# Performance work log

Hardware: AMD Instinct MI355X
Metric: run time of the kernel (lower is better)

## Reference

```python
import math
import jax, jax.numpy as jnp
import numpy as np

B, V, N, D = 256, 16, 1024, 512
CLIP = 10.0


def setup_inputs() -> dict:
    key = jax.random.key(0)
    ks = jax.random.split(key, 9)
    s = 0.02
    return {
        "g_node": jax.random.normal(ks[0], (B, D), jnp.float32),
        "Z_veh": jax.random.normal(ks[1], (B, V, D), jnp.float32),
        "g_graph": jax.random.normal(ks[2], (B, D), jnp.float32),
        "Z_node": jax.random.normal(ks[3], (B, N, D), jnp.float32),
        "mask": jax.random.randint(ks[4], (B, N), 0, 2).astype(bool),
        "W_ctx": jax.random.normal(ks[5], (D, 3 * D), jnp.float32) * s,
        "b_ctx": jnp.zeros((D,), jnp.float32),
        "Wq": jax.random.normal(ks[6], (D, D), jnp.float32) * s,
        "Wk": jax.random.normal(ks[7], (D, D), jnp.float32) * s,
    }


def reference(g_node, Z_veh, g_graph, Z_node, mask, W_ctx, b_ctx, Wq, Wk):
    scale = math.sqrt(Z_node.shape[-1])
    # concat -> Linear(3D, D) -> ReLU   (torch Linear: x @ W.T + b)
    cat = jnp.concatenate([g_node, Z_veh.mean(axis=1), g_graph], axis=-1)  # [B,3D]
    ctx = jax.nn.relu(cat @ W_ctx.T + b_ctx)  # [B,D]
    Q = ctx @ Wq.T  # [B,D]
    K = jnp.einsum("bnd,ed->bne", Z_node, Wk)  # [B,N,D]
    logits = jnp.einsum("bd,bnd->bn", Q, K) / scale  # [B,N]
    logits = CLIP * jnp.tanh(logits)
    logits = jnp.where(mask, logits, -jnp.inf)
    return logits
```

## Files before the change

### kernel.cpp

```cpp
#include <hip/hip_runtime.h>
#include <math.h>

#define Bz  256
#define Vz  16
#define Nz  1024
#define Dz  512
#define TD  1536
#define INV_SCALE 0.04419417382415922f
#define MASKED_VAL -1.0e30f

__global__ __launch_bounds__(256) void k0_zm(const float* __restrict__ Z_veh,
                                             float* __restrict__ Zm)
{
    const int idx = blockIdx.x * 256 + threadIdx.x;
    const int b   = idx >> 7;
    const int d4  = (idx & 127) * 4;
    const float* p = Z_veh + (size_t)b * Vz * Dz + d4;
    float4 s = {0.f, 0.f, 0.f, 0.f};
#pragma unroll
    for (int v = 0; v < Vz; ++v) {
        float4 t = *(const float4*)(p + (size_t)v * Dz);
        s.x += t.x; s.y += t.y; s.z += t.z; s.w += t.w;
    }
    s.x *= 0.0625f; s.y *= 0.0625f; s.z *= 0.0625f; s.w *= 0.0625f;
    *(float4*)&Zm[(size_t)b * Dz + d4] = s;
}

__global__ __launch_bounds__(256) void kA(const float* __restrict__ g_node,
                                          const float* __restrict__ Zm,
                                          const float* __restrict__ g_graph,
                                          const float* __restrict__ W_ctx,
                                          const float* __restrict__ Wq,
                                          const float* __restrict__ Wk,
                                          float* __restrict__ Cp2,
                                          float* __restrict__ GP)
{
    __shared__ float As[16][64];
    __shared__ float Bs[16][64];
    const int tid = threadIdx.x;
    const int tm = tid >> 4;
    const int tn = tid & 15;
    float acc[4][4] = {};

    if (blockIdx.x < 256) {
        const int idx = blockIdx.x;
        const int m0 = (idx >> 5) * 64;
        const int n0 = ((idx >> 3) & 3) * 64;
        const int kz = idx & 7;

        for (int kt = 0; kt < 192; kt += 16) {
            const int k0   = kz * 192 + kt;
            const int reg  = k0 >> 9;
            const int kloc = k0 & 511;
            const int ar = tid >> 2, ac = (tid & 3) * 4;
            float4 va = *(const float4*)&W_ctx[(size_t)(m0 + ar) * TD + k0 + ac];
            const int br = tid >> 2, bc = (tid & 3) * 4;
            const float* bsrc = (reg == 0) ? g_node : (reg == 2) ? g_graph : Zm;
            float4 vb = *(const float4*)&bsrc[(size_t)(n0 + br) * Dz + kloc + bc];
            __syncthreads();
            As[ac + 0][ar] = va.x; As[ac + 1][ar] = va.y;
            As[ac + 2][ar] = va.z; As[ac + 3][ar] = va.w;
            Bs[bc + 0][br] = vb.x; Bs[bc + 1][br] = vb.y;
            Bs[bc + 2][br] = vb.z; Bs[bc + 3][br] = vb.w;
            __syncthreads();
#pragma unroll
            for (int kk = 0; kk < 16; ++kk) {
                float4 a  = *(const float4*)&As[kk][tm * 4];
                float4 bb = *(const float4*)&Bs[kk][tn * 4];
                float av[4] = {a.x, a.y, a.z, a.w};
                float bv[4] = {bb.x, bb.y, bb.z, bb.w};
#pragma unroll
                for (int i = 0; i < 4; ++i)
#pragma unroll
                    for (int j = 0; j < 4; ++j)
                        acc[i][j] += av[i] * bv[j];
            }
        }
#pragma unroll
        for (int i = 0; i < 4; ++i) {
            float4 v = {acc[i][0], acc[i][1], acc[i][2], acc[i][3]};
            *(float4*)&Cp2[((size_t)kz * Dz + m0 + tm * 4 + i) * Bz + n0 + tn * 4] = v;
        }
    } else {
        const int g  = blockIdx.x - 256;
        const int m0 = (g >> 5) * 64;
        const int n0 = ((g >> 2) & 7) * 64;
        const int kz = g & 3;

        for (int kt = 0; kt < 128; kt += 16) {
            const int k0 = kz * 128 + kt;
            const int r = tid >> 4, c = (tid & 15) * 4;
            float4 va = *(const float4*)&Wq[(size_t)(k0 + r) * Dz + m0 + c];
            float4 vb = *(const float4*)&Wk[(size_t)(k0 + r) * Dz + n0 + c];
            __syncthreads();
            *(float4*)&As[r][c] = va;
            *(float4*)&Bs[r][c] = vb;
            __syncthreads();
#pragma unroll
            for (int kk = 0; kk < 16; ++kk) {
                float4 a  = *(const float4*)&As[kk][tm * 4];
                float4 bb = *(const float4*)&Bs[kk][tn * 4];
                float av[4] = {a.x, a.y, a.z, a.w};
                float bv[4] = {bb.x, bb.y, bb.z, bb.w};
#pragma unroll
                for (int i = 0; i < 4; ++i)
#pragma unroll
                    for (int j = 0; j < 4; ++j)
                        acc[i][j] += av[i] * bv[j];
            }
        }
#pragma unroll
        for (int i = 0; i < 4; ++i) {
            float4 v = {acc[i][0], acc[i][1], acc[i][2], acc[i][3]};
            *(float4*)&GP[((size_t)kz * Dz + m0 + tm * 4 + i) * Dz + n0 + tn * 4] = v;
        }
    }
}

__global__ __launch_bounds__(256) void kB(const float* __restrict__ Cp2,
                                          const float* __restrict__ bias,
                                          const float* __restrict__ GP,
                                          float* __restrict__ QkP)
{
    __shared__ float As[16][64];
    __shared__ float Bs[16][64];
    const int m0 = blockIdx.x * 64;
    const int n0 = blockIdx.y * 64;
    const int kz = blockIdx.z;
    const int tid = threadIdx.x;
    const int tm = tid >> 4, tn = tid & 15;

    float acc[4][4] = {};
    for (int kt = 0; kt < 64; kt += 16) {
        const int k0 = kz * 64 + kt;
        const int r = tid >> 4, col = (tid & 15) * 4;
        float4 s = {0.f, 0.f, 0.f, 0.f};
#pragma unroll
        for (int z = 0; z < 8; ++z) {
            float4 p = *(const float4*)&Cp2[((size_t)z * Dz + k0 + r) * Bz + m0 + col];
            s.x += p.x; s.y += p.y; s.z += p.z; s.w += p.w;
        }
        const float bv = bias[k0 + r];
        s.x = fmaxf(s.x + bv, 0.f); s.y = fmaxf(s.y + bv, 0.f);
        s.z = fmaxf(s.z + bv, 0.f); s.w = fmaxf(s.w + bv, 0.f);
        float4 t = {0.f, 0.f, 0.f, 0.f};
#pragma unroll
        for (int z = 0; z < 4; ++z) {
            float4 p = *(const float4*)&GP[((size_t)z * Dz + k0 + r) * Dz + n0 + col];
            t.x += p.x; t.y += p.y; t.z += p.z; t.w += p.w;
        }
        __syncthreads();
        *(float4*)&As[r][col] = s;
        *(float4*)&Bs[r][col] = t;
        __syncthreads();
#pragma unroll
        for (int kk = 0; kk < 16; ++kk) {
            float4 a  = *(const float4*)&As[kk][tm * 4];
            float4 bb = *(const float4*)&Bs[kk][tn * 4];
            float av[4] = {a.x, a.y, a.z, a.w};
            float bv2[4] = {bb.x, bb.y, bb.z, bb.w};
#pragma unroll
            for (int i = 0; i < 4; ++i)
#pragma unroll
                for (int j = 0; j < 4; ++j)
                    acc[i][j] += av[i] * bv2[j];
        }
    }
#pragma unroll
    for (int i = 0; i < 4; ++i) {
        float4 v = {acc[i][0], acc[i][1], acc[i][2], acc[i][3]};
        *(float4*)&QkP[((size_t)kz * Bz + m0 + tm * 4 + i) * Dz + n0 + tn * 4] = v;
    }
}

__global__ __launch_bounds__(256) void kC(const float* __restrict__ Z,
                                          const float* __restrict__ QkP,
                                          const unsigned char* __restrict__ mask,
                                          float* __restrict__ out)
{
    __shared__ float q_sh[Dz];
    const int b    = blockIdx.y;
    const int n0   = blockIdx.x * 64;
    const int tid  = threadIdx.x;

    {
        const int c2 = tid * 2;
        float2 s = {0.f, 0.f};
#pragma unroll
        for (int z = 0; z < 8; ++z) {
            float2 p = *(const float2*)&QkP[((size_t)z * Bz + b) * Dz + c2];
            s.x += p.x; s.y += p.y;
        }
        *(float2*)&q_sh[c2] = s;
    }
    __syncthreads();

    const int lane = tid & 63;
    const int wave = tid >> 6;
    const int grp  = lane >> 4;
    const int gl   = lane & 15;

    float4 q[8];
#pragma unroll
    for (int j = 0; j < 8; ++j)
        q[j] = *(const float4*)&q_sh[j * 64 + gl * 4];

    const float* zb = Z + ((size_t)b * Nz + n0) * Dz;

#pragma unroll
    for (int it = 0; it < 4; ++it) {
        const int r = wave * 16 + it * 4 + grp;
        const float* zp = zb + (size_t)r * Dz + gl * 4;
        float acc = 0.f;
#pragma unroll
        for (int j = 0; j < 8; ++j) {
            float4 z4 = *(const float4*)(zp + j * 64);
            acc += q[j].x * z4.x + q[j].y * z4.y + q[j].z * z4.z + q[j].w * z4.w;
        }
        acc += __shfl_xor(acc, 1, 64);
        acc += __shfl_xor(acc, 2, 64);
        acc += __shfl_xor(acc, 4, 64);
        acc += __shfl_xor(acc, 8, 64);
        if (gl == 0) {
            const int nn = n0 + r;
            float v = 10.0f * tanhf(acc * INV_SCALE);
            out[(size_t)b * Nz + nn] =
                mask[(size_t)b * Nz + nn] ? v : MASKED_VAL;
        }
    }
}

extern "C" void kernel_launch(void* const* d_in, const int* in_sizes, int n_in,
                              void* d_out, int out_size, void* d_ws, size_t ws_size,
                              hipStream_t stream)
{
    const float* g_node  = (const float*)d_in[0];
    const float* Z_veh   = (const float*)d_in[1];
    const float* g_graph = (const float*)d_in[2];
    const float* Z_node  = (const float*)d_in[3];
    const unsigned char* mask = (const unsigned char*)d_in[4];
    const float* W_ctx   = (const float*)d_in[5];
    const float* b_ctx   = (const float*)d_in[6];
    const float* Wq      = (const float*)d_in[7];
    const float* Wk      = (const float*)d_in[8];
    float* out = (float*)d_out;

    float* ws  = (float*)d_ws;
    float* Zm  = ws;
    float* Cp2 = ws + 131072;
    float* GP  = ws + 1179648;
    float* QkP = ws + 2228224;

    k0_zm<<<dim3(128), 256, 0, stream>>>(Z_veh, Zm);

    kA<<<dim3(512), 256, 0, stream>>>(g_node, Zm, g_graph, W_ctx, Wq, Wk,
                                      Cp2, GP);

    kB<<<dim3(4, 8, 8), 256, 0, stream>>>(Cp2, b_ctx, GP, QkP);

    kC<<<dim3(Nz / 64, Bz), 256, 0, stream>>>(Z_node, QkP, mask, out);
}
```

Baseline: 135.3 us.

## Merge the three prologue kernels into one cooperative kernel with grid syncs

Folds the Z_veh mean, the split-K context/weight GEMMs and the Q·Wk GEMM into a single cooperative launch of 512 blocks, with grid-wide barriers replacing kernel boundaries. The aim is to remove launch and inter-kernel drain overhead on the small prologue chain. In exchange it depends on all 512 blocks being co-resident for the cooperative launch, and grid.sync has its own cost. The last stage uses only 256 blocks, so half the grid sits idle there.

```diff
diff --git a/kernel.cpp b/kernel.cpp
--- a/kernel.cpp
+++ b/kernel.cpp
@@ -1,5 +1,8 @@
 #include <hip/hip_runtime.h>
+#include <hip/hip_cooperative_groups.h>
 #include <math.h>
+
+namespace cg = cooperative_groups;
 
 #define Bz  256
 #define Vz  16
@@ -9,167 +12,168 @@
 #define INV_SCALE 0.04419417382415922f
 #define MASKED_VAL -1.0e30f
 
-__global__ __launch_bounds__(256) void k0_zm(const float* __restrict__ Z_veh,
-                                             float* __restrict__ Zm)
+__global__ __launch_bounds__(256) void kChain(const float* __restrict__ g_node,
+                                              const float* __restrict__ Z_veh,
+                                              const float* __restrict__ g_graph,
+                                              const float* __restrict__ W_ctx,
+                                              const float* __restrict__ b_ctx,
+                                              const float* __restrict__ Wq,
+                                              const float* __restrict__ Wk,
+                                              float* __restrict__ Zm,
+                                              float* __restrict__ Cp2,
+                                              float* __restrict__ GP,
+                                              float* __restrict__ QkP)
 {
-    const int idx = blockIdx.x * 256 + threadIdx.x;
-    const int b   = idx >> 7;
-    const int d4  = (idx & 127) * 4;
-    const float* p = Z_veh + (size_t)b * Vz * Dz + d4;
-    float4 s = {0.f, 0.f, 0.f, 0.f};
-#pragma unroll
-    for (int v = 0; v < Vz; ++v) {
-        float4 t = *(const float4*)(p + (size_t)v * Dz);
-        s.x += t.x; s.y += t.y; s.z += t.z; s.w += t.w;
-    }
-    s.x *= 0.0625f; s.y *= 0.0625f; s.z *= 0.0625f; s.w *= 0.0625f;
-    *(float4*)&Zm[(size_t)b * Dz + d4] = s;
-}
-
-__global__ __launch_bounds__(256) void kA(const float* __restrict__ g_node,
-                                          const float* __restrict__ Zm,
-                                          const float* __restrict__ g_graph,
-                                          const float* __restrict__ W_ctx,
-                                          const float* __restrict__ Wq,
-                                          const float* __restrict__ Wk,
-                                          float* __restrict__ Cp2,
-                                          float* __restrict__ GP)
-{
+    cg::grid_group grid = cg::this_grid();
     __shared__ float As[16][64];
     __shared__ float Bs[16][64];
     const int tid = threadIdx.x;
     const int tm = tid >> 4;
     const int tn = tid & 15;
-    float acc[4][4] = {};
+
+    {
+        const int idx = blockIdx.x * 256 + tid;
+        if (idx < Bz * (Dz / 4)) {
+            const int b  = idx >> 7;
+            const int d4 = (idx & 127) * 4;
+            const float* p = Z_veh + (size_t)b * Vz * Dz + d4;
+            float4 s = {0.f, 0.f, 0.f, 0.f};
+#pragma unroll
+            for (int v = 0; v < Vz; ++v) {
+                float4 t = *(const float4*)(p + (size_t)v * Dz);
+                s.x += t.x; s.y += t.y; s.z += t.z; s.w += t.w;
+            }
+            s.x *= 0.0625f; s.y *= 0.0625f; s.z *= 0.0625f; s.w *= 0.0625f;
+            *(float4*)&Zm[(size_t)b * Dz + d4] = s;
+        }
+    }
+    grid.sync();
+
+    {
+        float acc[4][4] = {};
+        if (blockIdx.x < 256) {
+            const int idx = blockIdx.x;
+            const int m0 = (idx >> 5) * 64;
+            const int n0 = ((idx >> 3) & 3) * 64;
+            const int kz = idx & 7;
+
+            for (int kt = 0; kt < 192; kt += 16) {
+                const int k0   = kz * 192 + kt;
+                const int reg  = k0 >> 9;
+                const int kloc = k0 & 511;
+                const int ar = tid >> 2, ac = (tid & 3) * 4;
+                float4 va = *(const float4*)&W_ctx[(size_t)(m0 + ar) * TD + k0 + ac];
+                const int br = tid >> 2, bc = (tid & 3) * 4;
+                const float* bsrc = (reg == 0) ? g_node : (reg == 2) ? g_graph : Zm;
+                float4 vb = *(const float4*)&bsrc[(size_t)(n0 + br) * Dz + kloc + bc];
+                __syncthreads();
+                As[ac + 0][ar] = va.x; As[ac + 1][ar] = va.y;
+                As[ac + 2][ar] = va.z; As[ac + 3][ar] = va.w;
+                Bs[bc + 0][br] = vb.x; Bs[bc + 1][br] = vb.y;
+                Bs[bc + 2][br] = vb.z; Bs[bc + 3][br] = vb.w;
+                __syncthreads();
+#pragma unroll
+                for (int kk = 0; kk < 16; ++kk) {
+                    float4 a  = *(const float4*)&As[kk][tm * 4];
+                    float4 bb = *(const float4*)&Bs[kk][tn * 4];
+                    float av[4] = {a.x, a.y, a.z, a.w};
+                    float bv[4] = {bb.x, bb.y, bb.z, bb.w};
+#pragma unroll
+                    for (int i = 0; i < 4; ++i)
+#pragma unroll
+                        for (int j = 0; j < 4; ++j)
+                            acc[i][j] += av[i] * bv[j];
+                }
+            }
+#pragma unroll
+            for (int i = 0; i < 4; ++i) {
+                float4 v = {acc[i][0], acc[i][1], acc[i][2], acc[i][3]};
+                *(float4*)&Cp2[((size_t)kz * Dz + m0 + tm * 4 + i) * Bz + n0 + tn * 4] = v;
+            }
+        } else {
+            const int g  = blockIdx.x - 256;
+            const int m0 = (g >> 5) * 64;
+            const int n0 = ((g >> 2) & 7) * 64;
+            const int kz = g & 3;
+
+            for (int kt = 0; kt < 128; kt += 16) {
+                const int k0 = kz * 128 + kt;
+                const int r = tid >> 4, c = (tid & 15) * 4;
+                float4 va = *(const float4*)&Wq[(size_t)(k0 + r) * Dz + m0 + c];
+                float4 vb = *(const float4*)&Wk[(size_t)(k0 + r) * Dz + n0 + c];
+                __syncthreads();
+                *(float4*)&As[r][c] = va;
+                *(float4*)&Bs[r][c] = vb;
+                __syncthreads();
+#pragma unroll
+                for (int kk = 0; kk < 16; ++kk) {
+                    float4 a  = *(const float4*)&As[kk][tm * 4];
+                    float4 bb = *(const float4*)&Bs[kk][tn * 4];
+                    float av[4] = {a.x, a.y, a.z, a.w};
+                    float bv[4] = {bb.x, bb.y, bb.z, bb.w};
+#pragma unroll
+                    for (int i = 0; i < 4; ++i)
+#pragma unroll
+                        for (int j = 0; j < 4; ++j)
+                            acc[i][j] += av[i] * bv[j];
+                }
+            }
+#pragma unroll
+            for (int i = 0; i < 4; ++i) {
+                float4 v = {acc[i][0], acc[i][1], acc[i][2], acc[i][3]};
+                *(float4*)&GP[((size_t)kz * Dz + m0 + tm * 4 + i) * Dz + n0 + tn * 4] = v;
+            }
+        }
+    }
+    grid.sync();
 
     if (blockIdx.x < 256) {
-        const int idx = blockIdx.x;
-        const int m0 = (idx >> 5) * 64;
-        const int n0 = ((idx >> 3) & 3) * 64;
-        const int kz = idx & 7;
-
-        for (int kt = 0; kt < 192; kt += 16) {
-            const int k0   = kz * 192 + kt;
-            const int reg  = k0 >> 9;
-            const int kloc = k0 & 511;
-            const int ar = tid >> 2, ac = (tid & 3) * 4;
-            float4 va = *(const float4*)&W_ctx[(size_t)(m0 + ar) * TD + k0 + ac];
-            const int br = tid >> 2, bc = (tid & 3) * 4;
-            const float* bsrc = (reg == 0) ? g_node : (reg == 2) ? g_graph : Zm;
-            float4 vb = *(const float4*)&bsrc[(size_t)(n0 + br) * Dz + kloc + bc];
+        const int blk = blockIdx.x;
+        const int m0 = (blk & 3) * 64;
+        const int n0 = ((blk >> 2) & 7) * 64;
+        const int kz = blk >> 5;
+
+        float acc[4][4] = {};
+        for (int kt = 0; kt < 64; kt += 16) {
+            const int k0 = kz * 64 + kt;
+            const int r = tid >> 4, col = (tid & 15) * 4;
+            float4 s = {0.f, 0.f, 0.f, 0.f};
+#pragma unroll
+            for (int z = 0; z < 8; ++z) {
+                float4 p = *(const float4*)&Cp2[((size_t)z * Dz + k0 + r) * Bz + m0 + col];
+                s.x += p.x; s.y += p.y; s.z += p.z; s.w += p.w;
+            }
+            const float bv = b_ctx[k0 + r];
+            s.x = fmaxf(s.x + bv, 0.f); s.y = fmaxf(s.y + bv, 0.f);
+            s.z = fmaxf(s.z + bv, 0.f); s.w = fmaxf(s.w + bv, 0.f);
+            float4 t = {0.f, 0.f, 0.f, 0.f};
+#pragma unroll
+            for (int z = 0; z < 4; ++z) {
+                float4 p = *(const float4*)&GP[((size_t)z * Dz + k0 + r) * Dz + n0 + col];
+                t.x += p.x; t.y += p.y; t.z += p.z; t.w += p.w;
+            }
             __syncthreads();
-            As[ac + 0][ar] = va.x; As[ac + 1][ar] = va.y;
-            As[ac + 2][ar] = va.z; As[ac + 3][ar] = va.w;
-            Bs[bc + 0][br] = vb.x; Bs[bc + 1][br] = vb.y;
-            Bs[bc + 2][br] = vb.z; Bs[bc + 3][br] = vb.w;
+            *(float4*)&As[r][col] = s;
+            *(float4*)&Bs[r][col] = t;
             __syncthreads();
 #pragma unroll
             for (int kk = 0; kk < 16; ++kk) {
                 float4 a  = *(const float4*)&As[kk][tm * 4];
                 float4 bb = *(const float4*)&Bs[kk][tn * 4];
                 float av[4] = {a.x, a.y, a.z, a.w};
-                float bv[4] = {bb.x, bb.y, bb.z, bb.w};
+                float bv2[4] = {bb.x, bb.y, bb.z, bb.w};
 #pragma unroll
                 for (int i = 0; i < 4; ++i)
 #pragma unroll
                     for (int j = 0; j < 4; ++j)
-                        acc[i][j] += av[i] * bv[j];
+                        acc[i][j] += av[i] * bv2[j];
             }
         }
 #pragma unroll
         for (int i = 0; i < 4; ++i) {
             float4 v = {acc[i][0], acc[i][1], acc[i][2], acc[i][3]};
-            *(float4*)&Cp2[((size_t)kz * Dz + m0 + tm * 4 + i) * Bz + n0 + tn * 4] = v;
-        }
-    } else {
-        const int g  = blockIdx.x - 256;
-        const int m0 = (g >> 5) * 64;
-        const int n0 = ((g >> 2) & 7) * 64;
-        const int kz = g & 3;
-
-        for (int kt = 0; kt < 128; kt += 16) {
-            const int k0 = kz * 128 + kt;
-            const int r = tid >> 4, c = (tid & 15) * 4;
-            float4 va = *(const float4*)&Wq[(size_t)(k0 + r) * Dz + m0 + c];
-            float4 vb = *(const float4*)&Wk[(size_t)(k0 + r) * Dz + n0 + c];
-            __syncthreads();
-            *(float4*)&As[r][c] = va;
-            *(float4*)&Bs[r][c] = vb;
-            __syncthreads();
-#pragma unroll
-            for (int kk = 0; kk < 16; ++kk) {
-                float4 a  = *(const float4*)&As[kk][tm * 4];
-                float4 bb = *(const float4*)&Bs[kk][tn * 4];
-                float av[4] = {a.x, a.y, a.z, a.w};
-                float bv[4] = {bb.x, bb.y, bb.z, bb.w};
-#pragma unroll
-                for (int i = 0; i < 4; ++i)
-#pragma unroll
-                    for (int j = 0; j < 4; ++j)
-                        acc[i][j] += av[i] * bv[j];
-            }
-        }
-#pragma unroll
-        for (int i = 0; i < 4; ++i) {
-            float4 v = {acc[i][0], acc[i][1], acc[i][2], acc[i][3]};
-            *(float4*)&GP[((size_t)kz * Dz + m0 + tm * 4 + i) * Dz + n0 + tn * 4] = v;
-        }
-    }
-}
-
-__global__ __launch_bounds__(256) void kB(const float* __restrict__ Cp2,
-                                          const float* __restrict__ bias,
-                                          const float* __restrict__ GP,
-                                          float* __restrict__ QkP)
-{
-    __shared__ float As[16][64];
-    __shared__ float Bs[16][64];
-    const int m0 = blockIdx.x * 64;
-    const int n0 = blockIdx.y * 64;
-    const int kz = blockIdx.z;
-    const int tid = threadIdx.x;
-    const int tm = tid >> 4, tn = tid & 15;
-
-    float acc[4][4] = {};
-    for (int kt = 0; kt < 64; kt += 16) {
-        const int k0 = kz * 64 + kt;
-        const int r = tid >> 4, col = (tid & 15) * 4;
-        float4 s = {0.f, 0.f, 0.f, 0.f};
-#pragma unroll
-        for (int z = 0; z < 8; ++z) {
-            float4 p = *(const float4*)&Cp2[((size_t)z * Dz + k0 + r) * Bz + m0 + col];
-            s.x += p.x; s.y += p.y; s.z += p.z; s.w += p.w;
-        }
-        const float bv = bias[k0 + r];
-        s.x = fmaxf(s.x + bv, 0.f); s.y = fmaxf(s.y + bv, 0.f);
-        s.z = fmaxf(s.z + bv, 0.f); s.w = fmaxf(s.w + bv, 0.f);
-        float4 t = {0.f, 0.f, 0.f, 0.f};
-#pragma unroll
-        for (int z = 0; z < 4; ++z) {
-            float4 p = *(const float4*)&GP[((size_t)z * Dz + k0 + r) * Dz + n0 + col];
-            t.x += p.x; t.y += p.y; t.z += p.z; t.w += p.w;
-        }
-        __syncthreads();
-        *(float4*)&As[r][col] = s;
-        *(float4*)&Bs[r][col] = t;
-        __syncthreads();
-#pragma unroll
-        for (int kk = 0; kk < 16; ++kk) {
-            float4 a  = *(const float4*)&As[kk][tm * 4];
-            float4 bb = *(const float4*)&Bs[kk][tn * 4];
-            float av[4] = {a.x, a.y, a.z, a.w};
-            float bv2[4] = {bb.x, bb.y, bb.z, bb.w};
-#pragma unroll
-            for (int i = 0; i < 4; ++i)
-#pragma unroll
-                for (int j = 0; j < 4; ++j)
-                    acc[i][j] += av[i] * bv2[j];
-        }
-    }
-#pragma unroll
-    for (int i = 0; i < 4; ++i) {
-        float4 v = {acc[i][0], acc[i][1], acc[i][2], acc[i][3]};
-        *(float4*)&QkP[((size_t)kz * Bz + m0 + tm * 4 + i) * Dz + n0 + tn * 4] = v;
+            *(float4*)&QkP[((size_t)kz * Bz + m0 + tm * 4 + i) * Dz + n0 + tn * 4] = v;
+        }
     }
 }
 
@@ -251,12 +255,13 @@
     float* GP  = ws + 1179648;
     float* QkP = ws + 2228224;
 
-    k0_zm<<<dim3(128), 256, 0, stream>>>(Z_veh, Zm);
-
-    kA<<<dim3(512), 256, 0, stream>>>(g_node, Zm, g_graph, W_ctx, Wq, Wk,
-                                      Cp2, GP);
-
-    kB<<<dim3(4, 8, 8), 256, 0, stream>>>(Cp2, b_ctx, GP, QkP);
+    void* args[] = {
+        (void*)&g_node, (void*)&Z_veh, (void*)&g_graph, (void*)&W_ctx,
+        (void*)&b_ctx, (void*)&Wq, (void*)&Wk,
+        (void*)&Zm, (void*)&Cp2, (void*)&GP, (void*)&QkP
+    };
+    hipLaunchCooperativeKernel((void*)kChain, dim3(512), dim3(256),
+                               args, 0, stream);
 
     kC<<<dim3(Nz / 64, Bz), 256, 0, stream>>>(Z_node, QkP, mask, out);
 }
```

Result: slower. 255.7 us (+89.0%).
